# Kernel optimization log

Measured on AMD Instinct MI355X. Metric: run time of the kernel, lower is better.

The kernel has to match this reference:

```python
import jax, jax.numpy as jnp
import numpy as np

B, S, H, NH = 2, 1024, 1024, 16
SE, E = 512, 1024
NEXP, TOPK, FF = 8, 2, 2048
HD = H // NH
EPS = 1e-6
THETA = 10000.0
NEG = -1e9


def _rms(x, w):
    return x * jax.lax.rsqrt(jnp.mean(x * x, axis=-1, keepdims=True) + EPS) * w


def _rope(q, k, pos):
    # q,k: [B,S,NH,HD]; pos: [B,S] int
    inv = 1.0 / (THETA ** (jnp.arange(0, HD, 2, dtype=jnp.float32) / HD))
    f = pos[..., None].astype(jnp.float32) * inv            # [B,S,HD/2]
    emb = jnp.concatenate([f, f], axis=-1)                  # [B,S,HD]
    cos = jnp.cos(emb)[:, :, None, :]
    sin = jnp.sin(emb)[:, :, None, :]
    def rot(x):
        x1, x2 = jnp.split(x, 2, axis=-1)
        return jnp.concatenate([-x2, x1], axis=-1)
    return q * cos + rot(q) * sin, k * cos + rot(k) * sin


def _forward(hidden_states, encoder_hidden_states,
             in_ln_w, wq, wk, wv, wo,
             c_norm_w, cq_w, cq_b, ck_w, ck_b, cv_w, cv_b, co_w, co_b,
             post_ln_w, gate_w, w1, w2, w3,
             position_ids, encoder_attention_mask):
    x = hidden_states

    # ---- self-attention (RMSNorm pre-norm, RoPE, causal) ----
    res = x
    h = _rms(x, in_ln_w)
    q = (h @ wq.T).reshape(B, S, NH, HD)
    k = (h @ wk.T).reshape(B, S, NH, HD)
    v = (h @ wv.T).reshape(B, S, NH, HD)
    q, k = _rope(q, k, position_ids)
    scores = jnp.einsum('bqhd,bkhd->bhqk', q, k) / np.sqrt(HD)
    causal = jnp.tril(jnp.ones((S, S), dtype=bool))
    scores = jnp.where(causal, scores, NEG)
    attn = jax.nn.softmax(scores, axis=-1)
    o = jnp.einsum('bhqk,bkhd->bqhd', attn, v).reshape(B, S, H) @ wo.T
    x = res + o

    # ---- cross-attention block (RMSNorm, MHA with kdim=vdim=E, bias) ----
    res = x
    h = _rms(x, c_norm_w)
    cq = (h @ cq_w.T + cq_b).reshape(B, S, NH, HD)
    ck = (encoder_hidden_states @ ck_w.T + ck_b).reshape(B, SE, NH, HD)
    cv = (encoder_hidden_states @ cv_w.T + cv_b).reshape(B, SE, NH, HD)
    sc = jnp.einsum('bqhd,bkhd->bhqk', cq, ck) / np.sqrt(HD)
    pad = (encoder_attention_mask == 0)                     # key_padding_mask
    sc = jnp.where(pad[:, None, None, :], NEG, sc)
    ca = jax.nn.softmax(sc, axis=-1)
    o = jnp.einsum('bhqk,bkhd->bqhd', ca, cv).reshape(B, S, H) @ co_w.T + co_b
    x = res + o

    # ---- block-sparse MoE FFN (top-2 routing, SwiGLU experts) ----
    res = x
    h = _rms(x, post_ln_w).reshape(-1, H)                   # [T,H], T=B*S
    logits = h @ gate_w.T                                    # [T,NEXP]
    probs = jax.nn.softmax(logits, axis=-1)
    topv, topi = jax.lax.top_k(probs, TOPK)                  # [T,TOPK]
    topv = topv / jnp.sum(topv, axis=-1, keepdims=True)
    out = jnp.zeros_like(h)
    for e in range(NEXP):  # fixed small expert loop
        we = jnp.sum(jnp.where(topi == e, topv, 0.0), axis=-1)   # [T]
        ff = (jax.nn.silu(h @ w1[e].T) * (h @ w3[e].T)) @ w2[e].T
        out = out + we[:, None] * ff
    x = res + out.reshape(B, S, H)
    return x


def setup_inputs() -> dict:
    key = jax.random.key(0)
    ks = jax.random.split(key, 24)
    sc = 0.02
    d = {
        'hidden_states': jax.random.normal(ks[0], (B, S, H), jnp.float32),
        'position_ids': jnp.broadcast_to(jnp.arange(S, dtype=jnp.int64), (B, S)),
        'encoder_hidden_states': jax.random.normal(ks[1], (B, SE, E), jnp.float32),
        'encoder_attention_mask': jnp.ones((B, SE), jnp.int64),
        'in_ln_w': jnp.ones((H,), jnp.float32),
        'wq': jax.random.normal(ks[2], (H, H), jnp.float32) * sc,
        'wk': jax.random.normal(ks[3], (H, H), jnp.float32) * sc,
        'wv': jax.random.normal(ks[4], (H, H), jnp.float32) * sc,
        'wo': jax.random.normal(ks[5], (H, H), jnp.float32) * sc,
        'c_norm_w': jnp.ones((H,), jnp.float32),
        'cq_w': jax.random.normal(ks[6], (H, H), jnp.float32) * sc,
        'cq_b': jnp.zeros((H,), jnp.float32),
        'ck_w': jax.random.normal(ks[7], (H, E), jnp.float32) * sc,
        'ck_b': jnp.zeros((H,), jnp.float32),
        'cv_w': jax.random.normal(ks[8], (H, E), jnp.float32) * sc,
        'cv_b': jnp.zeros((H,), jnp.float32),
        'co_w': jax.random.normal(ks[9], (H, H), jnp.float32) * sc,
        'co_b': jnp.zeros((H,), jnp.float32),
        'post_ln_w': jnp.ones((H,), jnp.float32),
        'gate_w': jax.random.normal(ks[10], (NEXP, H), jnp.float32) * sc,
        'w1': jax.random.normal(ks[11], (NEXP, FF, H), jnp.float32) * sc,
        'w2': jax.random.normal(ks[12], (NEXP, H, FF), jnp.float32) * sc,
        'w3': jax.random.normal(ks[13], (NEXP, FF, H), jnp.float32) * sc,
    }
    return d


def reference(hidden_states, position_ids, encoder_hidden_states, encoder_attention_mask,
              in_ln_w, wq, wk, wv, wo,
              c_norm_w, cq_w, cq_b, ck_w, ck_b, cv_w, cv_b, co_w, co_b,
              post_ln_w, gate_w, w1, w2, w3):
    return _forward(hidden_states, encoder_hidden_states,
                    in_ln_w, wq, wk, wv, wo,
                    c_norm_w, cq_w, cq_b, ck_w, ck_b, cv_w, cv_b, co_w, co_b,
                    post_ln_w, gate_w, w1, w2, w3,
                    position_ids, encoder_attention_mask)
```

## Files before the change

kernel.cpp:

```cpp
#include <hip/hip_runtime.h>

#define B_    2
#define S_    1024
#define H_    1024
#define NH_   16
#define HD_   64
#define SE_   512
#define E_    1024
#define NEXP_ 8
#define FF_   2048
#define T_    (B_*S_)
#define TE_   (B_*SE_)
#define PERM_MAX 6400
#define MAXRT 24

typedef short v8s __attribute__((ext_vector_type(8)));
typedef short v4s __attribute__((ext_vector_type(4)));
typedef float v4f __attribute__((ext_vector_type(4)));
typedef _Float16 v8h __attribute__((ext_vector_type(8)));
typedef _Float16 v4h __attribute__((ext_vector_type(4)));

__device__ __forceinline__ unsigned short f2b(float f) {
  unsigned int u = __float_as_uint(f);
  u = (u + 0x7FFFu + ((u >> 16) & 1u)) >> 16;
  return (unsigned short)u;
}
__device__ __forceinline__ float b2f(unsigned short h) {
  return __uint_as_float(((unsigned int)h) << 16);
}

__device__ __forceinline__ void g2l16(const void* g, void* l) {
  __builtin_amdgcn_global_load_lds(
      (const __attribute__((address_space(1))) unsigned int*)g,
      (__attribute__((address_space(3))) unsigned int*)l, 16, 0, 0);
}

__global__ void detect_kern(const int* __restrict__ pos, const int* __restrict__ msk,
                            int* __restrict__ flags) {
  if (threadIdx.x == 0) {
    flags[0] = (pos[1] == 1) ? 0 : 1;
    flags[1] = (msk[1] == 1) ? 0 : 1;
  }
}

__global__ __launch_bounds__(256)
void split_kern(const float* __restrict__ x, _Float16* __restrict__ oh,
                _Float16* __restrict__ ol, int n8) {
  int i = blockIdx.x * 256 + threadIdx.x;
  if (i >= n8) return;
  v4f a = *(const v4f*)&x[i * 8];
  v4f b = *(const v4f*)&x[i * 8 + 4];
  v8h hv, lv;
  #pragma unroll
  for (int j = 0; j < 8; ++j) {
    float v = j < 4 ? a[j] : b[j - 4];
    _Float16 hh = (_Float16)v;
    hv[j] = hh; lv[j] = (_Float16)(v - (float)hh);
  }
  *(v8h*)&oh[i * 8] = hv;
  *(v8h*)&ol[i * 8] = lv;
}

__global__ __launch_bounds__(256)
void rmsnorm_hl_kern(const float* __restrict__ x, const float* __restrict__ w,
                     _Float16* __restrict__ yh, _Float16* __restrict__ yl) {
  int row = blockIdx.x, tid = threadIdx.x;
  const float* xr = x + (long)row * 1024;
  v4f v = *(const v4f*)&xr[tid * 4];
  float ss = v[0]*v[0] + v[1]*v[1] + v[2]*v[2] + v[3]*v[3];
  #pragma unroll
  for (int off = 32; off; off >>= 1) ss += __shfl_xor(ss, off);
  __shared__ float sw[4];
  if ((tid & 63) == 0) sw[tid >> 6] = ss;
  __syncthreads();
  float tot = sw[0] + sw[1] + sw[2] + sw[3];
  float rs = rsqrtf(tot * (1.0f / 1024.0f) + 1e-6f);
  const float* wr = w + tid * 4;
  v4h oh, ol;
  #pragma unroll
  for (int j = 0; j < 4; ++j) {
    float f = v[j] * rs * wr[j];
    _Float16 hh = (_Float16)f;
    oh[j] = hh; ol[j] = (_Float16)(f - (float)hh);
  }
  *(v4h*)&yh[(long)row * 1024 + tid * 4] = oh;
  *(v4h*)&yl[(long)row * 1024 + tid * 4] = ol;
}

__global__ __launch_bounds__(256)
void rmsnorm_kern(const float* __restrict__ x, const float* __restrict__ w,
                  unsigned short* __restrict__ y) {
  int row = blockIdx.x, tid = threadIdx.x;
  const float* xr = x + (long)row * 1024;
  v4f v = *(const v4f*)&xr[tid * 4];
  float ss = v[0]*v[0] + v[1]*v[1] + v[2]*v[2] + v[3]*v[3];
  #pragma unroll
  for (int off = 32; off; off >>= 1) ss += __shfl_xor(ss, off);
  __shared__ float sw[4];
  if ((tid & 63) == 0) sw[tid >> 6] = ss;
  __syncthreads();
  float tot = sw[0] + sw[1] + sw[2] + sw[3];
  float rs = rsqrtf(tot * (1.0f / 1024.0f) + 1e-6f);
  const float* wr = w + tid * 4;
  v4s o;
  #pragma unroll
  for (int j = 0; j < 4; ++j) o[j] = (short)f2b(v[j] * rs * wr[j]);
  *(v4s*)&y[(long)row * 1024 + tid * 4] = o;
}

__global__ __launch_bounds__(256)
void cvt_kern(const float* __restrict__ x, unsigned short* __restrict__ y, int n4) {
  int i = blockIdx.x * 256 + threadIdx.x;
  if (i >= n4) return;
  v4f v = *(const v4f*)&x[i * 4];
  v4s o;
  #pragma unroll
  for (int j = 0; j < 4; ++j) o[j] = (short)f2b(v[j]);
  *(v4s*)&y[i * 4] = o;
}

__global__ __launch_bounds__(256)
void rope_split_kern(float* __restrict__ q, const float* __restrict__ k,
                     _Float16* __restrict__ kh, _Float16* __restrict__ kl,
                     const int* __restrict__ pos, const int* __restrict__ flags) {
  int g = blockIdx.x * 256 + threadIdx.x;
  int d = g & 31;
  int h = (g >> 5) & 15;
  int s = (g >> 9) & (S_ - 1);
  int b = g >> 19;
  long base = (((long)(b * S_ + s)) * NH_ + h) * HD_;
  int pidx = b * S_ + s;
  int pv = pos[flags[0] ? (pidx << 1) : pidx];
  float p = (float)pv;
  float inv = powf(10000.0f, -(float)d * (1.0f / 32.0f));
  float f = p * inv;
  float sn = sinf(f), cs = cosf(f);
  float q1 = q[base + d], q2 = q[base + d + 32];
  q[base + d]      = q1 * cs - q2 * sn;
  q[base + d + 32] = q2 * cs + q1 * sn;
  float k1 = k[base + d], k2 = k[base + d + 32];
  float kr1 = k1 * cs - k2 * sn;
  float kr2 = k2 * cs + k1 * sn;
  _Float16 hh = (_Float16)kr1;
  kh[base + d] = hh; kl[base + d] = (_Float16)(kr1 - (float)hh);
  hh = (_Float16)kr2;
  kh[base + d + 32] = hh; kl[base + d + 32] = (_Float16)(kr2 - (float)hh);
}

__global__ __launch_bounds__(256)
void vtrans_kern(const float* __restrict__ vf, _Float16* __restrict__ vth,
                 _Float16* __restrict__ vtl, int Sk) {
  int kb = blockIdx.x, bh = blockIdx.y;
  int b = bh >> 4, h = bh & 15;
  int t = threadIdx.x;
  __shared__ float tile[64][65];
  int key = t >> 2, dsub = (t & 3) * 16;
  const float* src = vf + (((long)(b * Sk + kb * 64 + key)) * NH_ + h) * HD_ + dsub;
  #pragma unroll
  for (int j = 0; j < 16; j += 4) *(v4f*)&tile[key][dsub + j] = *(const v4f*)&src[j];
  __syncthreads();
  int d = t >> 2, ksub = (t & 3) * 16;
  v8h hv0, lv0, hv1, lv1;
  #pragma unroll
  for (int j = 0; j < 16; ++j) {
    float v = tile[ksub + j][d];
    _Float16 hh = (_Float16)v;
    if (j < 8) { hv0[j] = hh; lv0[j] = (_Float16)(v - (float)hh); }
    else       { hv1[j - 8] = hh; lv1[j - 8] = (_Float16)(v - (float)hh); }
  }
  long ob = (((long)(b * NH_ + h)) * HD_ + d) * Sk + kb * 64 + ksub;
  *(v8h*)&vth[ob] = hv0; *(v8h*)&vth[ob + 8] = hv1;
  *(v8h*)&vtl[ob] = lv0; *(v8h*)&vtl[ob + 8] = lv1;
}

struct ZArg {
  const _Float16 *Ah, *Al, *Bh, *Bl;
  const float *bias, *resid;
  float *Cf;
  _Float16 *Ch, *Cl;
  int M;
};

__global__ __launch_bounds__(256)
void gemm_hl(ZArg z0, ZArg z1, ZArg z2, int K) {
  ZArg za = blockIdx.z == 0 ? z0 : (blockIdx.z == 1 ? z1 : z2);
  int row0 = blockIdx.x * 128;
  if (row0 >= za.M) return;
  int col0 = blockIdx.y * 64;
  int tid = threadIdx.x, lane = tid & 63, w = tid >> 6;
  int lr = lane & 15, lg = lane >> 4;
  int wr = w >> 1, wc = w & 1;
  int rsw = (lr >> 1) & 3;

  __shared__ _Float16 Ah_s[128 * 32], Al_s[128 * 32];
  __shared__ _Float16 Bh_s[64 * 32], Bl_s[64 * 32];

  int av0 = w * 64 + lane, av1 = (w + 4) * 64 + lane;
  int ar0 = av0 >> 2, as0 = (av0 & 3) ^ ((ar0 >> 1) & 3);
  int ar1 = av1 >> 2, as1 = (av1 & 3) ^ ((ar1 >> 1) & 3);
  int bv = w * 64 + lane;
  int br = bv >> 2, bs = (bv & 3) ^ ((br >> 1) & 3);
  const _Float16* ga0h = za.Ah + (long)(row0 + ar0) * K + as0 * 8;
  const _Float16* ga0l = za.Al + (long)(row0 + ar0) * K + as0 * 8;
  const _Float16* ga1h = za.Ah + (long)(row0 + ar1) * K + as1 * 8;
  const _Float16* ga1l = za.Al + (long)(row0 + ar1) * K + as1 * 8;
  const _Float16* gbh  = za.Bh + (long)(col0 + br) * K + bs * 8;
  const _Float16* gbl  = za.Bl + (long)(col0 + br) * K + bs * 8;

  v4f acc[4][2] = {};

  for (int k0 = 0; k0 < K; k0 += 32) {
    __syncthreads();
    g2l16(ga0h + k0, (char*)Ah_s + w * 1024);
    g2l16(ga1h + k0, (char*)Ah_s + (w + 4) * 1024);
    g2l16(ga0l + k0, (char*)Al_s + w * 1024);
    g2l16(ga1l + k0, (char*)Al_s + (w + 4) * 1024);
    g2l16(gbh + k0, (char*)Bh_s + w * 1024);
    g2l16(gbl + k0, (char*)Bl_s + w * 1024);
    __syncthreads();

    v8h ah[4], al[4], bh[2], bl[2];
    #pragma unroll
    for (int m = 0; m < 4; ++m) {
      int off = (wr * 64 + m * 16 + lr) * 64 + ((lg ^ rsw) << 4);
      ah[m] = *(const v8h*)((char*)Ah_s + off);
      al[m] = *(const v8h*)((char*)Al_s + off);
    }
    #pragma unroll
    for (int n = 0; n < 2; ++n) {
      int off = (wc * 32 + n * 16 + lr) * 64 + ((lg ^ rsw) << 4);
      bh[n] = *(const v8h*)((char*)Bh_s + off);
      bl[n] = *(const v8h*)((char*)Bl_s + off);
    }
    #pragma unroll
    for (int m = 0; m < 4; ++m)
      #pragma unroll
      for (int n = 0; n < 2; ++n) {
        acc[m][n] = __builtin_amdgcn_mfma_f32_16x16x32_f16(ah[m], bh[n], acc[m][n], 0, 0, 0);
        acc[m][n] = __builtin_amdgcn_mfma_f32_16x16x32_f16(ah[m], bl[n], acc[m][n], 0, 0, 0);
        acc[m][n] = __builtin_amdgcn_mfma_f32_16x16x32_f16(al[m], bh[n], acc[m][n], 0, 0, 0);
      }
  }

  #pragma unroll
  for (int m = 0; m < 4; ++m) {
    int rbase = row0 + wr * 64 + m * 16 + lg * 4;
    #pragma unroll
    for (int n = 0; n < 2; ++n) {
      int gcol = col0 + wc * 32 + n * 16 + lr;
      float bb = za.bias ? za.bias[gcol] : 0.0f;
      #pragma unroll
      for (int rr = 0; rr < 4; ++rr) {
        long idx = (long)(rbase + rr) * 1024 + gcol;
        float v = acc[m][n][rr] + bb;
        if (za.Cf) {
          za.Cf[idx] = za.resid ? (za.resid[idx] + v) : v;
        } else {
          _Float16 hh = (_Float16)v;
          za.Ch[idx] = hh;
          za.Cl[idx] = (_Float16)(v - (float)hh);
        }
      }
    }
  }
}

template<bool CAUSAL>
__global__ __launch_bounds__(256)
void attn_hl(const float* __restrict__ Q,
             const _Float16* __restrict__ Khg, const _Float16* __restrict__ Klg,
             const _Float16* __restrict__ Vhg, const _Float16* __restrict__ Vlg,
             _Float16* __restrict__ Oh, _Float16* __restrict__ Ol,
             const int* __restrict__ mask, const int* __restrict__ flags,
             int Sq, int Sk, float qscale) {
  int qt = blockIdx.x, bh = blockIdx.y;
  int b = bh >> 4, h = bh & 15;
  int tid = threadIdx.x, lane = tid & 63, w = tid >> 6;
  int lr = lane & 15, lg = lane >> 4;
  int q0 = qt * 64;
  int mf = (!CAUSAL && mask) ? flags[1] : 0;
  int swz = lr & 7;

  __shared__ _Float16 Kh_s[64 * 64], Kl_s[64 * 64];
  __shared__ _Float16 Vh_s[64 * 64], Vl_s[64 * 64];
  __shared__ _Float16 Psh[4][16][72], Psl[4][16][72];

  v8h qh[2], ql[2];
  {
    long qbase = ((long)(b * Sq + q0 + w * 16 + lr) * NH_ + h) * HD_;
    #pragma unroll
    for (int kk = 0; kk < 2; ++kk) {
      v4f f0 = *(const v4f*)&Q[qbase + kk * 32 + lg * 8];
      v4f f1 = *(const v4f*)&Q[qbase + kk * 32 + lg * 8 + 4];
      #pragma unroll
      for (int j = 0; j < 8; ++j) {
        float f = (j < 4 ? f0[j] : f1[j - 4]) * qscale;
        _Float16 hh = (_Float16)f;
        qh[kk][j] = hh;
        ql[kk][j] = (_Float16)(f - (float)hh);
      }
    }
  }
  v4f of[4] = {};
  float m4[4], l4[4];
  #pragma unroll
  for (int i = 0; i < 4; ++i) { m4[i] = -3e38f; l4[i] = 0.0f; }

  int nkt = CAUSAL ? (qt + 1) : (Sk >> 6);
  for (int kt = 0; kt < nkt; ++kt) {
    __syncthreads();
    #pragma unroll
    for (int i = 0; i < 2; ++i) {
      int c = w + i * 4;
      int v = c * 64 + lane;
      int row = v >> 3, c8 = v & 7;
      int sc = (c8 ^ (row & 7)) << 3;
      long kb = ((long)(b * Sk + kt * 64 + row) * NH_ + h) * HD_ + sc;
      g2l16(Khg + kb, (char*)Kh_s + c * 1024);
      g2l16(Klg + kb, (char*)Kl_s + c * 1024);
      long vb = ((long)(b * NH_ + h) * HD_ + row) * Sk + kt * 64 + sc;
      g2l16(Vhg + vb, (char*)Vh_s + c * 1024);
      g2l16(Vlg + vb, (char*)Vl_s + c * 1024);
    }
    __syncthreads();

    v4f sf[4] = {};
    #pragma unroll
    for (int kk = 0; kk < 2; ++kk)
      #pragma unroll
      for (int n = 0; n < 4; ++n) {
        int off = (n * 16 + lr) * 128 + ((((kk << 2) | lg) ^ swz) << 4);
        v8h kbh = *(const v8h*)((char*)Kh_s + off);
        v8h kbl = *(const v8h*)((char*)Kl_s + off);
        sf[n] = __builtin_amdgcn_mfma_f32_16x16x32_f16(qh[kk], kbh, sf[n], 0, 0, 0);
        sf[n] = __builtin_amdgcn_mfma_f32_16x16x32_f16(qh[kk], kbl, sf[n], 0, 0, 0);
        sf[n] = __builtin_amdgcn_mfma_f32_16x16x32_f16(ql[kk], kbh, sf[n], 0, 0, 0);
      }

    if constexpr (CAUSAL) {
      if (kt == qt) {
        #pragma unroll
        for (int n = 0; n < 4; ++n) {
          int kcol = kt * 64 + n * 16 + lr;
          #pragma unroll
          for (int rr = 0; rr < 4; ++rr) {
            int qr = q0 + w * 16 + lg * 4 + rr;
            if (kcol > qr) sf[n][rr] = -1e9f;
          }
        }
      }
    } else {
      if (mask) {
        #pragma unroll
        for (int n = 0; n < 4; ++n) {
          int kcol = kt * 64 + n * 16 + lr;
          int mi = b * Sk + kcol;
          if (mask[mf ? (mi << 1) : mi] == 0) {
            #pragma unroll
            for (int rr = 0; rr < 4; ++rr) sf[n][rr] = -1e9f;
          }
        }
      }
    }

    float al[4];
    #pragma unroll
    for (int rr = 0; rr < 4; ++rr) {
      float mx = fmaxf(fmaxf(sf[0][rr], sf[1][rr]), fmaxf(sf[2][rr], sf[3][rr]));
      #pragma unroll
      for (int off = 8; off; off >>= 1) mx = fmaxf(mx, __shfl_xor(mx, off));
      float mn = fmaxf(m4[rr], mx);
      al[rr] = __expf(m4[rr] - mn);
      m4[rr] = mn;
      float rs = 0.0f;
      #pragma unroll
      for (int n = 0; n < 4; ++n) {
        float pv = __expf(sf[n][rr] - mn);
        sf[n][rr] = pv;
        rs += pv;
      }
      #pragma unroll
      for (int off = 8; off; off >>= 1) rs += __shfl_xor(rs, off);
      l4[rr] = l4[rr] * al[rr] + rs;
    }

    #pragma unroll
    for (int n = 0; n < 4; ++n)
      #pragma unroll
      for (int rr = 0; rr < 4; ++rr) {
        of[n][rr] *= al[rr];
        float pv = sf[n][rr];
        _Float16 ph = (_Float16)pv;
        Psh[w][lg * 4 + rr][n * 16 + lr] = ph;
        Psl[w][lg * 4 + rr][n * 16 + lr] = (_Float16)(pv - (float)ph);
      }
    __syncthreads();

    #pragma unroll
    for (int kc = 0; kc < 2; ++kc) {
      v8h pah = *(const v8h*)&Psh[w][lr][kc * 32 + lg * 8];
      v8h pal = *(const v8h*)&Psl[w][lr][kc * 32 + lg * 8];
      #pragma unroll
      for (int n = 0; n < 4; ++n) {
        int off = (n * 16 + lr) * 128 + ((((kc << 2) | lg) ^ swz) << 4);
        v8h vbh = *(const v8h*)((char*)Vh_s + off);
        v8h vbl = *(const v8h*)((char*)Vl_s + off);
        of[n] = __builtin_amdgcn_mfma_f32_16x16x32_f16(pah, vbh, of[n], 0, 0, 0);
        of[n] = __builtin_amdgcn_mfma_f32_16x16x32_f16(pah, vbl, of[n], 0, 0, 0);
        of[n] = __builtin_amdgcn_mfma_f32_16x16x32_f16(pal, vbh, of[n], 0, 0, 0);
      }
    }
  }

  #pragma unroll
  for (int rr = 0; rr < 4; ++rr) {
    int qr = q0 + w * 16 + lg * 4 + rr;
    float inv = 1.0f / l4[rr];
    long ob = (long)(b * Sq + qr) * 1024 + h * 64;
    #pragma unroll
    for (int n = 0; n < 4; ++n) {
      float v = of[n][rr] * inv;
      _Float16 hh = (_Float16)v;
      Oh[ob + n * 16 + lr] = hh;
      Ol[ob + n * 16 + lr] = (_Float16)(v - (float)hh);
    }
  }
}

__global__ __launch_bounds__(512)
void moe_gemm1(const unsigned short* __restrict__ A,
               const unsigned short* __restrict__ B1,
               const unsigned short* __restrict__ B2,
               unsigned short* __restrict__ Cb,
               const int* __restrict__ tm_e, const int* __restrict__ tm_slot,
               const int* __restrict__ ntl, const int* __restrict__ perm) {
  int tile = blockIdx.x;
  if (tile >= ntl[0]) return;
  int e = tm_e[tile];
  int row0 = tm_slot[tile];
  const unsigned short* Bp1 = B1 + (long)e * (FF_ * H_);
  const unsigned short* Bp2 = B2 + (long)e * (FF_ * H_);
  int col0 = blockIdx.y * 64;
  int tid = threadIdx.x, lane = tid & 63, w = tid >> 6;
  int lr = lane & 15, lg = lane >> 4;
  int wr = w >> 1, wc = w & 1;
  int rsw = (lr >> 1) & 3;

  __shared__ unsigned short As[256 * 32];
  __shared__ unsigned short Bs1[64 * 32];
  __shared__ unsigned short Bs2[64 * 32];

  const unsigned short* ga[2];
  #pragma unroll
  for (int i = 0; i < 2; ++i) {
    int c = i * 512 + tid;
    int r = c >> 2, sub = (c & 3) ^ ((r >> 1) & 3);
    int tok = perm[row0 + r];
    ga[i] = A + (long)(tok < 0 ? 0 : tok) * H_ + sub * 8;
  }
  int bc = tid & 255;
  int rb = bc >> 2, sb = (bc & 3) ^ ((rb >> 1) & 3);
  const unsigned short* gB = (tid < 256 ? Bp1 : Bp2) + (long)(col0 + rb) * H_ + sb * 8;
  unsigned short* lB = (tid < 256 ? Bs1 : Bs2) + (size_t)((w & 3) * 64) * 8;

  v4f acc[4][2] = {};
  v4f acc2[4][2] = {};

  for (int k0 = 0; k0 < H_; k0 += 32) {
    __syncthreads();
    #pragma unroll
    for (int i = 0; i < 2; ++i)
      g2l16(ga[i] + k0, As + (size_t)(i * 512 + w * 64) * 8);
    g2l16(gB + k0, lB);
    __syncthreads();

    v8s a[4], b1[2], b2[2];
    #pragma unroll
    for (int m = 0; m < 4; ++m)
      a[m] = *(const v8s*)&As[(wr * 64 + m * 16 + lr) * 32 + (lg ^ rsw) * 8];
    #pragma unroll
    for (int n = 0; n < 2; ++n) {
      b1[n] = *(const v8s*)&Bs1[(wc * 32 + n * 16 + lr) * 32 + (lg ^ rsw) * 8];
      b2[n] = *(const v8s*)&Bs2[(wc * 32 + n * 16 + lr) * 32 + (lg ^ rsw) * 8];
    }
    #pragma unroll
    for (int m = 0; m < 4; ++m)
      #pragma unroll
      for (int n = 0; n < 2; ++n) {
        acc[m][n]  = __builtin_amdgcn_mfma_f32_16x16x32_bf16(a[m], b1[n], acc[m][n], 0, 0, 0);
        acc2[m][n] = __builtin_amdgcn_mfma_f32_16x16x32_bf16(a[m], b2[n], acc2[m][n], 0, 0, 0);
      }
  }

  #pragma unroll
  for (int m = 0; m < 4; ++m) {
    int grow = row0 + wr * 64 + m * 16 + lg * 4;
    #pragma unroll
    for (int n = 0; n < 2; ++n) {
      int gcol = col0 + wc * 32 + n * 16 + lr;
      #pragma unroll
      for (int rr = 0; rr < 4; ++rr) {
        float v = acc[m][n][rr];
        float g = v / (1.0f + __expf(-v));
        Cb[(long)(grow + rr) * FF_ + gcol] = f2b(g * acc2[m][n][rr]);
      }
    }
  }
}

__global__ __launch_bounds__(512)
void moe_gemm2(const unsigned short* __restrict__ A,
               const unsigned short* __restrict__ B,
               float* __restrict__ Cf,
               const int* __restrict__ tm_e, const int* __restrict__ tm_slot,
               const int* __restrict__ ntl,
               const int* __restrict__ perm, const float* __restrict__ pwgt) {
  int tile = blockIdx.x;
  if (tile >= ntl[0]) return;
  int e = tm_e[tile];
  int row0 = tm_slot[tile];
  const unsigned short* Bp = B + (long)e * (H_ * FF_);
  int col0 = blockIdx.y * 128;
  int tid = threadIdx.x, lane = tid & 63, w = tid >> 6;
  int lr = lane & 15, lg = lane >> 4;
  int wr = w >> 1, wc = w & 1;
  int rsw = (lr >> 1) & 3;

  __shared__ unsigned short As[256 * 32];
  __shared__ unsigned short Bs[128 * 32];

  const unsigned short* ga[2];
  #pragma unroll
  for (int i = 0; i < 2; ++i) {
    int c = i * 512 + tid;
    int r = c >> 2, sub = (c & 3) ^ ((r >> 1) & 3);
    ga[i] = A + (long)(row0 + r) * FF_ + sub * 8;
  }
  int rb = tid >> 2, sb = (tid & 3) ^ ((rb >> 1) & 3);
  const unsigned short* gb = Bp + (long)(col0 + rb) * FF_ + sb * 8;

  v4f acc[4][4] = {};

  for (int k0 = 0; k0 < FF_; k0 += 32) {
    __syncthreads();
    #pragma unroll
    for (int i = 0; i < 2; ++i)
      g2l16(ga[i] + k0, As + (size_t)(i * 512 + w * 64) * 8);
    g2l16(gb + k0, Bs + (size_t)(w * 64) * 8);
    __syncthreads();

    v8s a[4], b[4];
    #pragma unroll
    for (int m = 0; m < 4; ++m)
      a[m] = *(const v8s*)&As[(wr * 64 + m * 16 + lr) * 32 + (lg ^ rsw) * 8];
    #pragma unroll
    for (int n = 0; n < 4; ++n)
      b[n] = *(const v8s*)&Bs[(wc * 64 + n * 16 + lr) * 32 + (lg ^ rsw) * 8];
    #pragma unroll
    for (int m = 0; m < 4; ++m)
      #pragma unroll
      for (int n = 0; n < 4; ++n)
        acc[m][n] = __builtin_amdgcn_mfma_f32_16x16x32_bf16(a[m], b[n], acc[m][n], 0, 0, 0);
  }

  #pragma unroll
  for (int m = 0; m < 4; ++m) {
    int grow = row0 + wr * 64 + m * 16 + lg * 4;
    #pragma unroll
    for (int rr = 0; rr < 4; ++rr) {
      int tok = perm[grow + rr];
      if (tok < 0) continue;
      float pw = pwgt[grow + rr];
      #pragma unroll
      for (int n = 0; n < 4; ++n) {
        int gcol = col0 + wc * 64 + n * 16 + lr;
        atomicAdd(&Cf[(long)tok * H_ + gcol], acc[m][n][rr] * pw);
      }
    }
  }
}

__global__ __launch_bounds__(64)
void router_kern(const float* __restrict__ x, const float* __restrict__ w,
                 const float* __restrict__ gw,
                 int* __restrict__ topi, float* __restrict__ topw,
                 int* __restrict__ counts) {
  int t = blockIdx.x, lane = threadIdx.x;
  const float* xr = x + (long)t * 1024;
  float vals[16];
  float ss = 0.0f;
  #pragma unroll
  for (int i = 0; i < 16; ++i) { float v = xr[lane + i * 64]; vals[i] = v; ss += v * v; }
  #pragma unroll
  for (int off = 32; off; off >>= 1) ss += __shfl_xor(ss, off);
  float rs = rsqrtf(ss * (1.0f / 1024.0f) + 1e-6f);
  #pragma unroll
  for (int i = 0; i < 16; ++i) vals[i] *= rs * w[lane + i * 64];
  float lgts[8];
  #pragma unroll
  for (int e = 0; e < 8; ++e) {
    const float* g = gw + e * 1024;
    float s = 0.0f;
    #pragma unroll
    for (int i = 0; i < 16; ++i) s += vals[i] * g[lane + i * 64];
    #pragma unroll
    for (int off = 32; off; off >>= 1) s += __shfl_xor(s, off);
    lgts[e] = s;
  }
  int i1 = 0; float l1 = lgts[0];
  #pragma unroll
  for (int e = 1; e < 8; ++e) if (lgts[e] > l1) { l1 = lgts[e]; i1 = e; }
  int i2 = -1; float l2 = -3e38f;
  #pragma unroll
  for (int e = 0; e < 8; ++e) if (e != i1 && lgts[e] > l2) { l2 = lgts[e]; i2 = e; }
  float w1 = 1.0f / (1.0f + __expf(l2 - l1));
  if (lane == 0) {
    topi[t * 2] = i1; topi[t * 2 + 1] = i2;
    topw[t * 2] = w1; topw[t * 2 + 1] = 1.0f - w1;
    atomicAdd(&counts[i1], 1);
    atomicAdd(&counts[i2], 1);
  }
}

__global__ __launch_bounds__(256)
void finalize_kern(const int* __restrict__ counts, int* __restrict__ poff,
                   int* __restrict__ tm_e, int* __restrict__ tm_slot,
                   int* __restrict__ ntl, int* __restrict__ perm) {
  __shared__ int stot;
  if (threadIdx.x == 0) {
    int off = 0, nt = 0;
    for (int e = 0; e < 8; ++e) {
      poff[e] = off;
      int c = counts[e];
      int ntE = (c + 255) >> 8;
      for (int i = 0; i < ntE; ++i) { tm_e[nt] = e; tm_slot[nt] = off + i * 256; ++nt; }
      off += ntE * 256;
    }
    ntl[0] = nt; ntl[1] = off;
    stot = off;
  }
  __syncthreads();
  for (int s = threadIdx.x; s < stot; s += 256) perm[s] = -1;
}

__global__ __launch_bounds__(256)
void scatter_kern(const int* __restrict__ topi, const float* __restrict__ topw,
                  const int* __restrict__ poff, int* __restrict__ cursor,
                  int* __restrict__ perm, float* __restrict__ pwgt) {
  int t = blockIdx.x * 256 + threadIdx.x;
  if (t >= T_) return;
  #pragma unroll
  for (int kk = 0; kk < 2; ++kk) {
    int e = topi[t * 2 + kk];
    int pos = atomicAdd(&cursor[e], 1);
    int slot = poff[e] + pos;
    perm[slot] = t;
    pwgt[slot] = topw[t * 2 + kk];
  }
}

extern "C" void kernel_launch(void* const* d_in, const int* in_sizes, int n_in,
                              void* d_out, int out_size, void* d_ws, size_t ws_size,
                              hipStream_t stream) {
  (void)in_sizes; (void)n_in; (void)out_size; (void)ws_size;
  const float* x_in  = (const float*)d_in[0];
  const int*  posids = (const int*)d_in[1];
  const float* enc   = (const float*)d_in[2];
  const int*  emask  = (const int*)d_in[3];
  const float* inln  = (const float*)d_in[4];
  const float* wq    = (const float*)d_in[5];
  const float* wk    = (const float*)d_in[6];
  const float* wv    = (const float*)d_in[7];
  const float* wo    = (const float*)d_in[8];
  const float* cnorm = (const float*)d_in[9];
  const float* cqw   = (const float*)d_in[10];
  const float* cqb   = (const float*)d_in[11];
  const float* ckw   = (const float*)d_in[12];
  const float* ckb   = (const float*)d_in[13];
  const float* cvw   = (const float*)d_in[14];
  const float* cvb   = (const float*)d_in[15];
  const float* cow   = (const float*)d_in[16];
  const float* cob   = (const float*)d_in[17];
  const float* pln   = (const float*)d_in[18];
  const float* gatew = (const float*)d_in[19];
  const float* w1    = (const float*)d_in[20];
  const float* w2    = (const float*)d_in[21];
  const float* w3    = (const float*)d_in[22];
  float* out = (float*)d_out;

  char* p = (char*)d_ws;
  auto alloc = [&](size_t bytes) -> char* {
    char* r = p;
    p += (bytes + 255) & ~(size_t)255;
    return r;
  };
  const size_t MB = 1024 * 1024;
  char* A1 = alloc(4 * MB);
  char* A2 = alloc(4 * MB);
  char* Bq = alloc(8 * MB);
  char* Bk = alloc(8 * MB);
  char* Bv = alloc(8 * MB);
  char* C1 = alloc(4 * MB);
  char* C2 = alloc(4 * MB);
  char* D1 = alloc(4 * MB);
  char* D2 = alloc(4 * MB);
  float* x1 = (float*)alloc(8 * MB);
  float* x2 = (float*)alloc(8 * MB);
  unsigned short* h3b = (unsigned short*)alloc(4 * MB);
  _Float16* ench = (_Float16*)alloc(2 * MB);
  _Float16* encl = (_Float16*)alloc(2 * MB);
  int*   meta    = (int*)alloc(4 * (8 + 8 + 8 + 2 + 2 + MAXRT + MAXRT));
  int*   counts  = meta;
  int*   cursor  = meta + 8;
  int*   poff    = meta + 16;
  int*   ntl     = meta + 24;
  int*   flags   = meta + 26;
  int*   tm_e    = meta + 28;
  int*   tm_slot = meta + 28 + MAXRT;
  int*   topi    = (int*)alloc((size_t)T_ * 2 * 4);
  float* topw    = (float*)alloc((size_t)T_ * 2 * 4);
  int*   perm    = (int*)alloc((size_t)PERM_MAX * 4);
  float* pwgt    = (float*)alloc((size_t)PERM_MAX * 4);
  unsigned short* w1b = (unsigned short*)alloc((size_t)NEXP_ * FF_ * H_ * 2);
  unsigned short* w3b = (unsigned short*)alloc((size_t)NEXP_ * FF_ * H_ * 2);
  unsigned short* w2b = (unsigned short*)alloc((size_t)NEXP_ * H_ * FF_ * 2);

  _Float16 *hh = (_Float16*)A1, *hl = (_Float16*)A2;
  _Float16 *oh = (_Float16*)A1, *ol = (_Float16*)A2;
  _Float16 *ckh = (_Float16*)A1, *ckl = (_Float16*)A2;
  float* qf = (float*)Bq;  float* cqf = (float*)Bq;
  float* kf = (float*)Bk;
  _Float16 *cvth = (_Float16*)Bk, *cvtl = (_Float16*)(Bk + 4 * MB);
  float* vf = (float*)Bv;  float* cvf = (float*)Bv;
  _Float16 *kh = (_Float16*)C1, *kl = (_Float16*)C2;
  _Float16 *h2h = (_Float16*)C1, *h2l = (_Float16*)C2;
  _Float16 *vth = (_Float16*)D1, *vtl = (_Float16*)D2;
  _Float16 *coh = (_Float16*)D1, *col = (_Float16*)D2;
  unsigned short* ffh = (unsigned short*)Bq;
  _Float16* wsp = (_Float16*)w1b;
  auto wsph = [&](int i) { return wsp + (size_t)i * 2097152; };
  auto wspl = [&](int i) { return wsp + (size_t)i * 2097152 + 1048576; };

  dim3 blk(256);
  const int WN8 = H_ * H_ / 8;

  detect_kern<<<1, 64, 0, stream>>>(posids, emask, flags);

  const float* wlist[8] = {wq, wk, wv, wo, cqw, ckw, cvw, cow};
  for (int i = 0; i < 8; ++i)
    split_kern<<<(WN8 + 255) / 256, blk, 0, stream>>>(wlist[i], wsph(i), wspl(i), WN8);
  split_kern<<<(TE_ * E_ / 8 + 255) / 256, blk, 0, stream>>>(enc, ench, encl, TE_ * E_ / 8);

  rmsnorm_hl_kern<<<T_, blk, 0, stream>>>(x_in, inln, hh, hl);
  {
    ZArg zq = {hh, hl, wsph(0), wspl(0), nullptr, nullptr, qf, nullptr, nullptr, 2048};
    ZArg zk = {hh, hl, wsph(1), wspl(1), nullptr, nullptr, kf, nullptr, nullptr, 2048};
    ZArg zv = {hh, hl, wsph(2), wspl(2), nullptr, nullptr, vf, nullptr, nullptr, 2048};
    gemm_hl<<<dim3(16, 16, 3), blk, 0, stream>>>(zq, zk, zv, 1024);
  }
  rope_split_kern<<<(B_ * S_ * NH_ * 32) / 256, blk, 0, stream>>>(qf, kf, kh, kl, posids, flags);
  vtrans_kern<<<dim3(16, 32), blk, 0, stream>>>(vf, vth, vtl, 1024);
  attn_hl<true><<<dim3(16, 32), blk, 0, stream>>>(
      qf, kh, kl, vth, vtl, oh, ol, nullptr, flags, 1024, 1024, 0.125f);
  {
    ZArg zo = {oh, ol, wsph(3), wspl(3), nullptr, x_in, x1, nullptr, nullptr, 2048};
    gemm_hl<<<dim3(16, 16, 1), blk, 0, stream>>>(zo, zo, zo, 1024);
  }

  rmsnorm_hl_kern<<<T_, blk, 0, stream>>>(x1, cnorm, h2h, h2l);
  {
    ZArg zcq = {h2h, h2l, wsph(4), wspl(4), cqb, nullptr, cqf, nullptr, nullptr, 2048};
    ZArg zck = {ench, encl, wsph(5), wspl(5), ckb, nullptr, nullptr, ckh, ckl, 1024};
    ZArg zcv = {ench, encl, wsph(6), wspl(6), cvb, nullptr, cvf, nullptr, nullptr, 1024};
    gemm_hl<<<dim3(16, 16, 3), blk, 0, stream>>>(zcq, zck, zcv, 1024);
  }
  vtrans_kern<<<dim3(8, 32), blk, 0, stream>>>(cvf, cvth, cvtl, 512);
  attn_hl<false><<<dim3(16, 32), blk, 0, stream>>>(
      cqf, ckh, ckl, cvth, cvtl, coh, col, emask, flags, 1024, 512, 0.125f);
  {
    ZArg zco = {coh, col, wsph(7), wspl(7), cob, x1, x2, nullptr, nullptr, 2048};
    gemm_hl<<<dim3(16, 16, 1), blk, 0, stream>>>(zco, zco, zco, 1024);
  }

  cvt_kern<<<(NEXP_ * FF_ * H_ / 4 + 255) / 256, blk, 0, stream>>>(w1, w1b, NEXP_ * FF_ * H_ / 4);
  cvt_kern<<<(NEXP_ * FF_ * H_ / 4 + 255) / 256, blk, 0, stream>>>(w3, w3b, NEXP_ * FF_ * H_ / 4);
  cvt_kern<<<(NEXP_ * H_ * FF_ / 4 + 255) / 256, blk, 0, stream>>>(w2, w2b, NEXP_ * H_ * FF_ / 4);
  rmsnorm_kern<<<T_, blk, 0, stream>>>(x2, pln, h3b);
  hipMemsetAsync(meta, 0, 64, stream);
  router_kern<<<T_, dim3(64), 0, stream>>>(x2, pln, gatew, topi, topw, counts);
  finalize_kern<<<1, blk, 0, stream>>>(counts, poff, tm_e, tm_slot, ntl, perm);
  scatter_kern<<<(T_ + 255) / 256, blk, 0, stream>>>(topi, topw, poff, cursor, perm, pwgt);
  moe_gemm1<<<dim3(MAXRT, FF_ / 64), dim3(512), 0, stream>>>(
      h3b, w1b, w3b, ffh, tm_e, tm_slot, ntl, perm);
  hipMemcpyAsync(out, x2, (size_t)T_ * H_ * 4, hipMemcpyDeviceToDevice, stream);
  moe_gemm2<<<dim3(MAXRT, H_ / 128), dim3(512), 0, stream>>>(
      ffh, w2b, out, tm_e, tm_slot, ntl, perm, pwgt);
}
```

Baseline: 593.8 us.

## Double-buffer LDS tiles in GEMM kernels and halve MoE gemm2 column tile

```diff
diff --git a/kernel.cpp b/kernel.cpp
--- a/kernel.cpp
+++ b/kernel.cpp
@@ -192,8 +192,8 @@
   int wr = w >> 1, wc = w & 1;
   int rsw = (lr >> 1) & 3;
 
-  __shared__ _Float16 Ah_s[128 * 32], Al_s[128 * 32];
-  __shared__ _Float16 Bh_s[64 * 32], Bl_s[64 * 32];
+  __shared__ _Float16 Ah_s[2][128 * 32], Al_s[2][128 * 32];
+  __shared__ _Float16 Bh_s[2][64 * 32], Bl_s[2][64 * 32];
 
   int av0 = w * 64 + lane, av1 = (w + 4) * 64 + lane;
   int ar0 = av0 >> 2, as0 = (av0 & 3) ^ ((ar0 >> 1) & 3);
@@ -207,30 +207,35 @@
   const _Float16* gbh  = za.Bh + (long)(col0 + br) * K + bs * 8;
   const _Float16* gbl  = za.Bl + (long)(col0 + br) * K + bs * 8;
 
+  auto stage = [&](int buf, int k0) {
+    g2l16(ga0h + k0, (char*)Ah_s[buf] + w * 1024);
+    g2l16(ga1h + k0, (char*)Ah_s[buf] + (w + 4) * 1024);
+    g2l16(ga0l + k0, (char*)Al_s[buf] + w * 1024);
+    g2l16(ga1l + k0, (char*)Al_s[buf] + (w + 4) * 1024);
+    g2l16(gbh + k0, (char*)Bh_s[buf] + w * 1024);
+    g2l16(gbl + k0, (char*)Bl_s[buf] + w * 1024);
+  };
+
   v4f acc[4][2] = {};
+  stage(0, 0);
+  int cur = 0;
 
   for (int k0 = 0; k0 < K; k0 += 32) {
     __syncthreads();
-    g2l16(ga0h + k0, (char*)Ah_s + w * 1024);
-    g2l16(ga1h + k0, (char*)Ah_s + (w + 4) * 1024);
-    g2l16(ga0l + k0, (char*)Al_s + w * 1024);
-    g2l16(ga1l + k0, (char*)Al_s + (w + 4) * 1024);
-    g2l16(gbh + k0, (char*)Bh_s + w * 1024);
-    g2l16(gbl + k0, (char*)Bl_s + w * 1024);
-    __syncthreads();
+    if (k0 + 32 < K) stage(cur ^ 1, k0 + 32);
 
     v8h ah[4], al[4], bh[2], bl[2];
     #pragma unroll
     for (int m = 0; m < 4; ++m) {
       int off = (wr * 64 + m * 16 + lr) * 64 + ((lg ^ rsw) << 4);
-      ah[m] = *(const v8h*)((char*)Ah_s + off);
-      al[m] = *(const v8h*)((char*)Al_s + off);
+      ah[m] = *(const v8h*)((char*)Ah_s[cur] + off);
+      al[m] = *(const v8h*)((char*)Al_s[cur] + off);
     }
     #pragma unroll
     for (int n = 0; n < 2; ++n) {
       int off = (wc * 32 + n * 16 + lr) * 64 + ((lg ^ rsw) << 4);
-      bh[n] = *(const v8h*)((char*)Bh_s + off);
-      bl[n] = *(const v8h*)((char*)Bl_s + off);
+      bh[n] = *(const v8h*)((char*)Bh_s[cur] + off);
+      bl[n] = *(const v8h*)((char*)Bl_s[cur] + off);
     }
     #pragma unroll
     for (int m = 0; m < 4; ++m)
@@ -240,6 +245,7 @@
         acc[m][n] = __builtin_amdgcn_mfma_f32_16x16x32_f16(ah[m], bl[n], acc[m][n], 0, 0, 0);
         acc[m][n] = __builtin_amdgcn_mfma_f32_16x16x32_f16(al[m], bh[n], acc[m][n], 0, 0, 0);
       }
+    cur ^= 1;
   }
 
   #pragma unroll
@@ -446,9 +452,9 @@
   int wr = w >> 1, wc = w & 1;
   int rsw = (lr >> 1) & 3;
 
-  __shared__ unsigned short As[256 * 32];
-  __shared__ unsigned short Bs1[64 * 32];
-  __shared__ unsigned short Bs2[64 * 32];
+  __shared__ unsigned short As[2][256 * 32];
+  __shared__ unsigned short Bs1[2][64 * 32];
+  __shared__ unsigned short Bs2[2][64 * 32];
 
   const unsigned short* ga[2];
   #pragma unroll
@@ -461,27 +467,32 @@
   int bc = tid & 255;
   int rb = bc >> 2, sb = (bc & 3) ^ ((rb >> 1) & 3);
   const unsigned short* gB = (tid < 256 ? Bp1 : Bp2) + (long)(col0 + rb) * H_ + sb * 8;
-  unsigned short* lB = (tid < 256 ? Bs1 : Bs2) + (size_t)((w & 3) * 64) * 8;
+  size_t lBoff = (size_t)((w & 3) * 64) * 8;
+
+  auto stage = [&](int buf, int k0) {
+    #pragma unroll
+    for (int i = 0; i < 2; ++i)
+      g2l16(ga[i] + k0, As[buf] + (size_t)(i * 512 + w * 64) * 8);
+    g2l16(gB + k0, (tid < 256 ? Bs1[buf] : Bs2[buf]) + lBoff);
+  };
 
   v4f acc[4][2] = {};
   v4f acc2[4][2] = {};
+  stage(0, 0);
+  int cur = 0;
 
   for (int k0 = 0; k0 < H_; k0 += 32) {
     __syncthreads();
-    #pragma unroll
-    for (int i = 0; i < 2; ++i)
-      g2l16(ga[i] + k0, As + (size_t)(i * 512 + w * 64) * 8);
-    g2l16(gB + k0, lB);
-    __syncthreads();
+    if (k0 + 32 < H_) stage(cur ^ 1, k0 + 32);
 
     v8s a[4], b1[2], b2[2];
     #pragma unroll
     for (int m = 0; m < 4; ++m)
-      a[m] = *(const v8s*)&As[(wr * 64 + m * 16 + lr) * 32 + (lg ^ rsw) * 8];
+      a[m] = *(const v8s*)&As[cur][(wr * 64 + m * 16 + lr) * 32 + (lg ^ rsw) * 8];
     #pragma unroll
     for (int n = 0; n < 2; ++n) {
-      b1[n] = *(const v8s*)&Bs1[(wc * 32 + n * 16 + lr) * 32 + (lg ^ rsw) * 8];
-      b2[n] = *(const v8s*)&Bs2[(wc * 32 + n * 16 + lr) * 32 + (lg ^ rsw) * 8];
+      b1[n] = *(const v8s*)&Bs1[cur][(wc * 32 + n * 16 + lr) * 32 + (lg ^ rsw) * 8];
+      b2[n] = *(const v8s*)&Bs2[cur][(wc * 32 + n * 16 + lr) * 32 + (lg ^ rsw) * 8];
     }
     #pragma unroll
     for (int m = 0; m < 4; ++m)
@@ -490,6 +501,7 @@
         acc[m][n]  = __builtin_amdgcn_mfma_f32_16x16x32_bf16(a[m], b1[n], acc[m][n], 0, 0, 0);
         acc2[m][n] = __builtin_amdgcn_mfma_f32_16x16x32_bf16(a[m], b2[n], acc2[m][n], 0, 0, 0);
       }
+    cur ^= 1;
   }
 
   #pragma unroll
@@ -520,14 +532,14 @@
   int e = tm_e[tile];
   int row0 = tm_slot[tile];
   const unsigned short* Bp = B + (long)e * (H_ * FF_);
-  int col0 = blockIdx.y * 128;
+  int col0 = blockIdx.y * 64;
   int tid = threadIdx.x, lane = tid & 63, w = tid >> 6;
   int lr = lane & 15, lg = lane >> 4;
   int wr = w >> 1, wc = w & 1;
   int rsw = (lr >> 1) & 3;
 
-  __shared__ unsigned short As[256 * 32];
-  __shared__ unsigned short Bs[128 * 32];
+  __shared__ unsigned short As[2][256 * 32];
+  __shared__ unsigned short Bs[2][64 * 32];
 
   const unsigned short* ga[2];
   #pragma unroll
@@ -536,31 +548,39 @@
     int r = c >> 2, sub = (c & 3) ^ ((r >> 1) & 3);
     ga[i] = A + (long)(row0 + r) * FF_ + sub * 8;
   }
-  int rb = tid >> 2, sb = (tid & 3) ^ ((rb >> 1) & 3);
+  int bc = tid & 255;
+  int rb = bc >> 2, sb = (bc & 3) ^ ((rb >> 1) & 3);
   const unsigned short* gb = Bp + (long)(col0 + rb) * FF_ + sb * 8;
-
-  v4f acc[4][4] = {};
+  size_t lBoff = (size_t)((w & 3) * 64) * 8;
+
+  auto stage = [&](int buf, int k0) {
+    #pragma unroll
+    for (int i = 0; i < 2; ++i)
+      g2l16(ga[i] + k0, As[buf] + (size_t)(i * 512 + w * 64) * 8);
+    if (tid < 256) g2l16(gb + k0, Bs[buf] + lBoff);
+  };
+
+  v4f acc[4][2] = {};
+  stage(0, 0);
+  int cur = 0;
 
   for (int k0 = 0; k0 < FF_; k0 += 32) {
     __syncthreads();
-    #pragma unroll
-    for (int i = 0; i < 2; ++i)
-      g2l16(ga[i] + k0, As + (size_t)(i * 512 + w * 64) * 8);
-    g2l16(gb + k0, Bs + (size_t)(w * 64) * 8);
-    __syncthreads();
-
-    v8s a[4], b[4];
+    if (k0 + 32 < FF_) stage(cur ^ 1, k0 + 32);
+
+    v8s a[4], b[2];
     #pragma unroll
     for (int m = 0; m < 4; ++m)
-      a[m] = *(const v8s*)&As[(wr * 64 + m * 16 + lr) * 32 + (lg ^ rsw) * 8];
-    #pragma unroll
-    for (int n = 0; n < 4; ++n)
-      b[n] = *(const v8s*)&Bs[(wc * 64 + n * 16 + lr) * 32 + (lg ^ rsw) * 8];
+      a[m] = *(const v8s*)&As[cur][(wr * 64 + m * 16 + lr) * 32 + (lg ^ rsw) * 8];
+    #pragma unroll
+    for (int n = 0; n < 2; ++n)
+      b[n] = *(const v8s*)&Bs[cur][(wc * 32 + n * 16 + lr) * 32 + (lg ^ rsw) * 8];
     #pragma unroll
     for (int m = 0; m < 4; ++m)
       #pragma unroll
-      for (int n = 0; n < 4; ++n)
+      for (int n = 0; n < 2; ++n)
         acc[m][n] = __builtin_amdgcn_mfma_f32_16x16x32_bf16(a[m], b[n], acc[m][n], 0, 0, 0);
+    cur ^= 1;
   }
 
   #pragma unroll
@@ -572,8 +592,8 @@
       if (tok < 0) continue;
       float pw = pwgt[grow + rr];
       #pragma unroll
-      for (int n = 0; n < 4; ++n) {
-        int gcol = col0 + wc * 64 + n * 16 + lr;
+      for (int n = 0; n < 2; ++n) {
+        int gcol = col0 + wc * 32 + n * 16 + lr;
         atomicAdd(&Cf[(long)tok * H_ + gcol], acc[m][n][rr] * pw);
       }
     }
@@ -793,6 +813,6 @@
   moe_gemm1<<<dim3(MAXRT, FF_ / 64), dim3(512), 0, stream>>>(
       h3b, w1b, w3b, ffh, tm_e, tm_slot, ntl, perm);
   hipMemcpyAsync(out, x2, (size_t)T_ * H_ * 4, hipMemcpyDeviceToDevice, stream);
-  moe_gemm2<<<dim3(MAXRT, H_ / 128), dim3(512), 0, stream>>>(
+  moe_gemm2<<<dim3(MAXRT, H_ / 64), dim3(512), 0, stream>>>(
       ffh, w2b, out, tm_e, tm_slot, ntl, perm, pwgt);
 }
```

New measurement: 579.5 us. 1.02x faster.
